# Kernel optimization log

Measured on AMD Instinct MI355X. Metric: run time of the kernel, lower is better.

## Reference

```python
import jax, jax.numpy as jnp
import numpy as np

HID = 2048      # hidden_size
NH = 32         # num_heads
G = 8           # num_kv_groups
R = NH // G     # repeat factor (heads per kv group)
HD = HID // NH  # head_dim = 64
SCALE = HD ** 0.5


def setup_inputs() -> dict:
    key = jax.random.key(0)
    ks = jax.random.split(key, 10)
    B, S = 2, 1024
    x = jax.random.normal(ks[0], (B, S, HID), dtype=jnp.float32)
    attention_mask = jnp.ones((B, S, S), dtype=jnp.float32)
    # Linear params stored as [in, out] (y = x @ W + b), same math as torch Linear.
    Wq = jax.random.normal(ks[1], (HID, HID), dtype=jnp.float32) * 0.02
    bq = jnp.zeros((HID,), dtype=jnp.float32)
    Wk = jax.random.normal(ks[2], (HID, G * HD), dtype=jnp.float32) * 0.02
    bk = jnp.zeros((G * HD,), dtype=jnp.float32)
    Wv = jax.random.normal(ks[3], (HID, G * HD), dtype=jnp.float32) * 0.02
    bv = jnp.zeros((G * HD,), dtype=jnp.float32)
    Wo = jax.random.normal(ks[4], (HID, HID), dtype=jnp.float32) * 0.02
    bo = jnp.zeros((HID,), dtype=jnp.float32)
    return {"x": x, "attention_mask": attention_mask,
            "Wq": Wq, "bq": bq, "Wk": Wk, "bk": bk,
            "Wv": Wv, "bv": bv, "Wo": Wo, "bo": bo}


def reference(x, attention_mask, Wq, bq, Wk, bk, Wv, bv, Wo, bo):
    B, S, _ = x.shape
    # Projections. Group heads as (G, R) instead of repeat_interleave:
    # repeat_interleave(key, R, dim=2) duplicates each kv group R times, which is
    # exactly sharing key[:, :, g] across the R heads of group g.
    q = (x @ Wq + bq).reshape(B, S, G, R, HD)   # [B,S,G,R,HD] (heads = G*R in order)
    k = (x @ Wk + bk).reshape(B, S, G, HD)      # [B,S,G,HD]
    v = (x @ Wv + bv).reshape(B, S, G, HD)
    # scores [B,G,R,Sq,Sk] == torch's [B, NH, Sq, Sk] with NH = G*R
    scores = jnp.einsum('bqgrd,bkgd->bgrqk', q, k) / SCALE
    scores = scores * attention_mask[:, None, None]  # multiplicative mask per head
    w = jax.nn.softmax(scores, axis=-1)
    out = jnp.einsum('bgrqk,bkgd->bqgrd', w, v).reshape(B, S, HID)
    return out @ Wo + bo + x
```

## Files before the change

### kernel.cpp

```cpp
#include <hip/hip_runtime.h>

typedef unsigned short u16;
typedef unsigned int u32;
typedef __attribute__((ext_vector_type(8))) short bf16x8;
typedef __attribute__((ext_vector_type(4))) float f32x4;

#define HID 2048
#define S_LEN 1024
#define BATCH 2
#define G_KV 8
#define R_REP 4
#define HD 64
#define NQKV 3072

__device__ __forceinline__ u16 f2bf(float f) {
    union { u32 u; float ff; } x; x.ff = f;
    u32 u = x.u;
    u += 0x7FFFu + ((u >> 16) & 1u);
    return (u16)(u >> 16);
}
__device__ __forceinline__ float bf2f(u16 v) {
    union { u32 u; float f; } x; x.u = ((u32)v) << 16; return x.f;
}

__device__ __forceinline__ void gload_lds16(const void* g, void* l) {
    __builtin_amdgcn_global_load_lds((const __attribute__((address_space(1))) void*)g,
                                     (__attribute__((address_space(3))) void*)l,
                                     16, 0, 0);
}

__global__ __launch_bounds__(256) void cvt_x(const float* __restrict__ in,
                                             u16* __restrict__ out) {
    int i = (blockIdx.x * 256 + threadIdx.x) * 8;
    float4 a = *(const float4*)(in + i);
    float4 b = *(const float4*)(in + i + 4);
    u16 t[8] = {f2bf(a.x), f2bf(a.y), f2bf(a.z), f2bf(a.w),
                f2bf(b.x), f2bf(b.y), f2bf(b.z), f2bf(b.w)};
    *(uint4*)(out + i) = *(const uint4*)t;
}

__global__ __launch_bounds__(256) void mask_perm(const float* __restrict__ mask,
                                                 u16* __restrict__ out) {
    __shared__ float tile[64 * 68];
    int bid = blockIdx.x;
    int kt = bid & 15, qblk = (bid >> 4) & 15, b = bid >> 8;
    int t = threadIdx.x;
    int row = t >> 2, c0 = (t & 3) * 16;
    const float* src = mask + ((size_t)b * S_LEN + qblk * 64 + row) * S_LEN + kt * 64 + c0;
#pragma unroll
    for (int i = 0; i < 4; ++i)
        *(float4*)&tile[row * 68 + c0 + i * 4] = *(const float4*)(src + i * 4);
    __syncthreads();
    int w = t >> 6, quad = (t >> 4) & 3, l16 = t & 15;
    int prow = w * 16 + quad * 4;
    u16 v[16];
#pragma unroll
    for (int nt = 0; nt < 4; ++nt)
#pragma unroll
        for (int reg = 0; reg < 4; ++reg)
            v[nt * 4 + reg] = f2bf(tile[(prow + reg) * 68 + nt * 16 + l16]);
    u16* dst = out + ((size_t)bid) * 4096 + t * 16;
    *(uint4*)dst = ((uint4*)v)[0];
    *(uint4*)(dst + 8) = ((uint4*)v)[1];
}

__global__ __launch_bounds__(256) void transpose_qkv(const float* __restrict__ Wq,
                                                     const float* __restrict__ Wk,
                                                     const float* __restrict__ Wv,
                                                     u16* __restrict__ out) {
    __shared__ float tile[32][33];
    int n0 = blockIdx.x * 32, k0 = blockIdx.y * 32;
    const float* in; int N, nc0;
    if (n0 < 2048)      { in = Wq; N = 2048; nc0 = n0; }
    else if (n0 < 2560) { in = Wk; N = 512;  nc0 = n0 - 2048; }
    else                { in = Wv; N = 512;  nc0 = n0 - 2560; }
    int tx = threadIdx.x, ty = threadIdx.y;
#pragma unroll
    for (int j = 0; j < 4; ++j)
        tile[ty + j * 8][tx] = in[(size_t)(k0 + ty + j * 8) * N + nc0 + tx];
    __syncthreads();
#pragma unroll
    for (int j = 0; j < 4; ++j)
        out[(size_t)(n0 + ty + j * 8) * 2048 + k0 + tx] = f2bf(tile[tx][ty + j * 8]);
}

__global__ __launch_bounds__(256) void transpose_cvt(const float* __restrict__ in,
                                                     u16* __restrict__ out,
                                                     int K, int N) {
    __shared__ float tile[32][33];
    int n0 = blockIdx.x * 32, k0 = blockIdx.y * 32;
    int tx = threadIdx.x, ty = threadIdx.y;
#pragma unroll
    for (int j = 0; j < 4; ++j)
        tile[ty + j * 8][tx] = in[(size_t)(k0 + ty + j * 8) * N + n0 + tx];
    __syncthreads();
#pragma unroll
    for (int j = 0; j < 4; ++j)
        out[(size_t)(n0 + ty + j * 8) * K + k0 + tx] = f2bf(tile[tx][ty + j * 8]);
}

__global__ __launch_bounds__(256) void gemm_qkv(const u16* __restrict__ Xb,
                                                const u16* __restrict__ WT,
                                                const float* __restrict__ bq,
                                                const float* __restrict__ bk,
                                                const float* __restrict__ bv,
                                                u16* __restrict__ qb,
                                                u16* __restrict__ kb,
                                                u16* __restrict__ vb) {
    __shared__ __align__(16) u16 As[64 * 32];
    __shared__ __align__(16) u16 Bs[128 * 32];
    int tid = threadIdx.x;
    int w = tid >> 6, lane = tid & 63, quad = lane >> 4, l16 = lane & 15;
    int m0 = blockIdx.y * 64, n0 = blockIdx.x * 128;
    int wr = (w >> 1) * 32, wc = (w & 1) * 64;
    int srow = lane >> 2, scol = (lane & 3) * 8;

    f32x4 acc[2][4];
#pragma unroll
    for (int i = 0; i < 2; ++i)
#pragma unroll
        for (int j = 0; j < 4; ++j) acc[i][j] = (f32x4){0.f, 0.f, 0.f, 0.f};

    for (int k0 = 0; k0 < 2048; k0 += 32) {
        gload_lds16(&Xb[(size_t)(m0 + w * 16 + srow) * 2048 + k0 + scol], &As[(w * 16) * 32]);
#pragma unroll
        for (int c = 0; c < 2; ++c) {
            int row = w * 32 + c * 16;
            gload_lds16(&WT[(size_t)(n0 + row + srow) * 2048 + k0 + scol], &Bs[row * 32]);
        }
        __syncthreads();
        bf16x8 af[2], bfr[4];
#pragma unroll
        for (int mt = 0; mt < 2; ++mt)
            af[mt] = *(const bf16x8*)&As[(wr + mt * 16 + l16) * 32 + quad * 8];
#pragma unroll
        for (int nt = 0; nt < 4; ++nt)
            bfr[nt] = *(const bf16x8*)&Bs[(wc + nt * 16 + l16) * 32 + quad * 8];
#pragma unroll
        for (int mt = 0; mt < 2; ++mt)
#pragma unroll
            for (int nt = 0; nt < 4; ++nt)
                acc[mt][nt] = __builtin_amdgcn_mfma_f32_16x16x32_bf16(af[mt], bfr[nt], acc[mt][nt], 0, 0, 0);
        __syncthreads();
    }

#pragma unroll
    for (int nt = 0; nt < 4; ++nt) {
        int n = n0 + wc + nt * 16 + l16;
        float bias;
        if (n < 2048) bias = bq[n];
        else if (n < 2560) bias = bk[n - 2048];
        else bias = bv[n - 2560];
#pragma unroll
        for (int mt = 0; mt < 2; ++mt) {
#pragma unroll
            for (int reg = 0; reg < 4; ++reg) {
                int m = m0 + wr + mt * 16 + quad * 4 + reg;
                float val = acc[mt][nt][reg] + bias;
                int b = m >> 10, s = m & 1023;
                if (n < 2048) {
                    int g = n >> 8, r = (n >> 6) & 3, d = n & 63;
                    qb[((((size_t)(b * G_KV + g) * R_REP + r) * S_LEN) + s) * HD + d] = f2bf(val * 0.125f);
                } else if (n < 2560) {
                    int n2 = n - 2048, g = n2 >> 6, d = n2 & 63;
                    kb[(((size_t)(b * G_KV + g) * S_LEN) + s) * HD + d] = f2bf(val);
                } else {
                    int n2 = n - 2560, g = n2 >> 6, d = n2 & 63;
                    vb[(((size_t)(b * G_KV + g) * HD + d) * S_LEN) + s] = f2bf(val);
                }
            }
        }
    }
}

__global__ __launch_bounds__(256) void attn_mfma(const u16* __restrict__ qbuf,
                                                 const u16* __restrict__ kbuf,
                                                 const u16* __restrict__ vtbuf,
                                                 const u16* __restrict__ mask_pm,
                                                 u16* __restrict__ aout) {
    __shared__ __align__(16) u16 Ks[64 * 72];
    __shared__ __align__(16) u16 Vs[64 * 72];
    __shared__ __align__(16) u16 Ps[64 * 72];

    int d = blockIdx.x;
    int xcd = d & 7, j = d >> 3;
    int pr = xcd * 2 + (j >> 6);
    int r = (j >> 4) & 3, qblk = j & 15;
    int b = pr >> 3, g = pr & 7;

    int tid = threadIdx.x;
    int w = tid >> 6, lane = tid & 63, quad = lane >> 4, l16 = lane & 15;
    int s0 = qblk * 64;

    const u16* qrow = qbuf +
        ((((size_t)(b * G_KV + g) * R_REP + r) * S_LEN) + s0 + w * 16 + l16) * HD;
    bf16x8 qf0 = *(const bf16x8*)(qrow + quad * 8);
    bf16x8 qf1 = *(const bf16x8*)(qrow + 32 + quad * 8);

    f32x4 o_acc[4];
#pragma unroll
    for (int i = 0; i < 4; ++i) o_acc[i] = (f32x4){0.f, 0.f, 0.f, 0.f};
    float l_tot[4] = {0.f, 0.f, 0.f, 0.f};

    const u16* kbase  = kbuf  + (size_t)(b * G_KV + g) * S_LEN * HD;
    const u16* vtbase = vtbuf + (size_t)(b * G_KV + g) * HD * S_LEN;
    const u16* mbase  = mask_pm + ((size_t)(b * 16 + qblk) * 16) * 4096 + tid * 16;

    int srow = tid >> 2, sc = (tid & 3) * 16;
    int prow = w * 16 + quad * 4;

    uint4 kp0, kp1, vp0, vp1, mp0, mp1;
    {
        const u16* kr = kbase + (size_t)srow * HD + sc;
        kp0 = *(const uint4*)kr; kp1 = *(const uint4*)(kr + 8);
        const u16* vr = vtbase + (size_t)srow * S_LEN + sc;
        vp0 = *(const uint4*)vr; vp1 = *(const uint4*)(vr + 8);
        mp0 = *(const uint4*)mbase; mp1 = *(const uint4*)(mbase + 8);
    }

    for (int kt = 0; kt < 16; ++kt) {
        __syncthreads();
        *(uint4*)&Ks[srow * 72 + sc]     = kp0;
        *(uint4*)&Ks[srow * 72 + sc + 8] = kp1;
        *(uint4*)&Vs[srow * 72 + sc]     = vp0;
        *(uint4*)&Vs[srow * 72 + sc + 8] = vp1;
        uint4 m0c = mp0, m1c = mp1;
        __syncthreads();

        if (kt < 15) {
            int nk = (kt + 1) * 64;
            const u16* kr = kbase + (size_t)(nk + srow) * HD + sc;
            kp0 = *(const uint4*)kr; kp1 = *(const uint4*)(kr + 8);
            const u16* vr = vtbase + (size_t)srow * S_LEN + nk + sc;
            vp0 = *(const uint4*)vr; vp1 = *(const uint4*)(vr + 8);
            const u16* mr = mbase + (size_t)(kt + 1) * 4096;
            mp0 = *(const uint4*)mr; mp1 = *(const uint4*)(mr + 8);
        }

        f32x4 p[4];
#pragma unroll
        for (int nt = 0; nt < 4; ++nt) {
            bf16x8 kf0 = *(const bf16x8*)&Ks[(nt * 16 + l16) * 72 + quad * 8];
            bf16x8 kf1 = *(const bf16x8*)&Ks[(nt * 16 + l16) * 72 + 32 + quad * 8];
            f32x4 z = (f32x4){0.f, 0.f, 0.f, 0.f};
            z = __builtin_amdgcn_mfma_f32_16x16x32_bf16(qf0, kf0, z, 0, 0, 0);
            p[nt] = __builtin_amdgcn_mfma_f32_16x16x32_bf16(qf1, kf1, z, 0, 0, 0);
        }

        const u16* mv0 = (const u16*)&m0c;
        const u16* mv1 = (const u16*)&m1c;
        float part[4] = {0.f, 0.f, 0.f, 0.f};
#pragma unroll
        for (int nt = 0; nt < 4; ++nt) {
#pragma unroll
            for (int reg = 0; reg < 4; ++reg) {
                int idx = nt * 4 + reg;
                float m = bf2f(idx < 8 ? mv0[idx] : mv1[idx - 8]);
                float e = __expf(p[nt][reg] * m);
                part[reg] += e;
                Ps[(prow + reg) * 72 + nt * 16 + l16] = f2bf(e);
            }
        }
        __syncthreads();

#pragma unroll
        for (int reg = 0; reg < 4; ++reg) {
            float v = part[reg];
            v += __shfl_xor(v, 1);
            v += __shfl_xor(v, 2);
            v += __shfl_xor(v, 4);
            v += __shfl_xor(v, 8);
            l_tot[reg] += v;
        }

        bf16x8 pf0 = *(const bf16x8*)&Ps[(w * 16 + l16) * 72 + quad * 8];
        bf16x8 pf1 = *(const bf16x8*)&Ps[(w * 16 + l16) * 72 + 32 + quad * 8];
#pragma unroll
        for (int nt = 0; nt < 4; ++nt) {
            bf16x8 vf0 = *(const bf16x8*)&Vs[(nt * 16 + l16) * 72 + quad * 8];
            bf16x8 vf1 = *(const bf16x8*)&Vs[(nt * 16 + l16) * 72 + 32 + quad * 8];
            o_acc[nt] = __builtin_amdgcn_mfma_f32_16x16x32_bf16(pf0, vf0, o_acc[nt], 0, 0, 0);
            o_acc[nt] = __builtin_amdgcn_mfma_f32_16x16x32_bf16(pf1, vf1, o_acc[nt], 0, 0, 0);
        }
    }

#pragma unroll
    for (int reg = 0; reg < 4; ++reg) {
        int row = prow + reg;
        float inv = 1.0f / l_tot[reg];
        int sidx = s0 + row;
        u16* dst = aout + ((size_t)(b * S_LEN + sidx)) * HID + (g * R_REP + r) * HD;
#pragma unroll
        for (int nt = 0; nt < 4; ++nt)
            dst[nt * 16 + l16] = f2bf(o_acc[nt][reg] * inv);
    }
}

__global__ __launch_bounds__(256) void gemm_o(const u16* __restrict__ A,
                                              const u16* __restrict__ WT,
                                              const float* __restrict__ bo,
                                              const float* __restrict__ Xres,
                                              float* __restrict__ out) {
    __shared__ __align__(16) u16 As[64 * 32];
    __shared__ __align__(16) u16 Bs[128 * 32];
    int tid = threadIdx.x;
    int w = tid >> 6, lane = tid & 63, quad = lane >> 4, l16 = lane & 15;
    int m0 = blockIdx.y * 64, n0 = blockIdx.x * 128;
    int wr = (w >> 1) * 32, wc = (w & 1) * 64;
    int srow = lane >> 2, scol = (lane & 3) * 8;

    f32x4 acc[2][4];
#pragma unroll
    for (int i = 0; i < 2; ++i)
#pragma unroll
        for (int j = 0; j < 4; ++j) acc[i][j] = (f32x4){0.f, 0.f, 0.f, 0.f};

    for (int k0 = 0; k0 < 2048; k0 += 32) {
        gload_lds16(&A[(size_t)(m0 + w * 16 + srow) * 2048 + k0 + scol], &As[(w * 16) * 32]);
#pragma unroll
        for (int c = 0; c < 2; ++c) {
            int row = w * 32 + c * 16;
            gload_lds16(&WT[(size_t)(n0 + row + srow) * 2048 + k0 + scol], &Bs[row * 32]);
        }
        __syncthreads();
        bf16x8 af[2], bfr[4];
#pragma unroll
        for (int mt = 0; mt < 2; ++mt)
            af[mt] = *(const bf16x8*)&As[(wr + mt * 16 + l16) * 32 + quad * 8];
#pragma unroll
        for (int nt = 0; nt < 4; ++nt)
            bfr[nt] = *(const bf16x8*)&Bs[(wc + nt * 16 + l16) * 32 + quad * 8];
#pragma unroll
        for (int mt = 0; mt < 2; ++mt)
#pragma unroll
            for (int nt = 0; nt < 4; ++nt)
                acc[mt][nt] = __builtin_amdgcn_mfma_f32_16x16x32_bf16(af[mt], bfr[nt], acc[mt][nt], 0, 0, 0);
        __syncthreads();
    }

#pragma unroll
    for (int nt = 0; nt < 4; ++nt) {
        int n = n0 + wc + nt * 16 + l16;
        float bias = bo[n];
#pragma unroll
        for (int mt = 0; mt < 2; ++mt) {
#pragma unroll
            for (int reg = 0; reg < 4; ++reg) {
                int m = m0 + wr + mt * 16 + quad * 4 + reg;
                out[(size_t)m * 2048 + n] = acc[mt][nt][reg] + bias + Xres[(size_t)m * 2048 + n];
            }
        }
    }
}

extern "C" void kernel_launch(void* const* d_in, const int* in_sizes, int n_in,
                              void* d_out, int out_size, void* d_ws, size_t ws_size,
                              hipStream_t stream) {
    const float* x    = (const float*)d_in[0];
    const float* mask = (const float*)d_in[1];
    const float* Wq   = (const float*)d_in[2];
    const float* bq   = (const float*)d_in[3];
    const float* Wk   = (const float*)d_in[4];
    const float* bk   = (const float*)d_in[5];
    const float* Wv   = (const float*)d_in[6];
    const float* bv   = (const float*)d_in[7];
    const float* Wo   = (const float*)d_in[8];
    const float* bo   = (const float*)d_in[9];
    float* out = (float*)d_out;

    u16* ws = (u16*)d_ws;
    size_t off = 0;
    u16* WqkvT = ws + off; off += (size_t)NQKV * 2048;
    u16* WoT   = ws + off; off += (size_t)2048 * 2048;
    u16* q_buf = ws + off; off += (size_t)BATCH * G_KV * R_REP * S_LEN * HD;
    u16* k_buf = ws + off; off += (size_t)BATCH * G_KV * S_LEN * HD;
    u16* v_buf = ws + off; off += (size_t)BATCH * G_KV * S_LEN * HD;
    u16* a_out = ws + off; off += (size_t)2048 * 2048;
    u16* Xb      = a_out;
    u16* mask_pm = WqkvT;

    cvt_x<<<dim3(2048 * 2048 / (256 * 8)), 256, 0, stream>>>(x, Xb);

    dim3 tb(32, 8);
    transpose_qkv<<<dim3(96, 64), tb, 0, stream>>>(Wq, Wk, Wv, WqkvT);
    transpose_cvt<<<dim3(64, 64), tb, 0, stream>>>(Wo, WoT, 2048, 2048);

    gemm_qkv<<<dim3(NQKV / 128, 2048 / 64), 256, 0, stream>>>(Xb, WqkvT, bq, bk, bv,
                                                              q_buf, k_buf, v_buf);

    mask_perm<<<dim3(BATCH * 16 * 16), 256, 0, stream>>>(mask, mask_pm);

    attn_mfma<<<dim3(BATCH * G_KV * R_REP * (S_LEN / 64)), 256, 0, stream>>>(
        q_buf, k_buf, v_buf, mask_pm, a_out);

    gemm_o<<<dim3(2048 / 128, 2048 / 64), 256, 0, stream>>>(a_out, WoT, bo, x, out);
}
```

Measured before the change: 249.4 us.

## Compute transposed S tile so P is written packed without intra-block barrier

The QK^T MFMA now swaps operands so each lane holds scores for one query row across four consecutive keys. This lets the exp results be rounded and packed into bf16 pairs and written to LDS with one 8-byte store per tile instead of scalar stores. The per-iteration row-sum shuffles go away: each lane accumulates a private partial, which is reduced once at the end through shuffles and a small LDS array, and the __syncthreads before reading P is dropped because each wave only reads its own rows. The mask is kept as fp32 in the new permuted layout, which doubles mask traffic and register use. The end-of-kernel LDS read of row sums has no barrier, which is safe only if each wave reads only the rows it wrote.

```diff
diff --git a/kernel.cpp b/kernel.cpp
--- a/kernel.cpp
+++ b/kernel.cpp
@@ -18,9 +18,6 @@
     u32 u = x.u;
     u += 0x7FFFu + ((u >> 16) & 1u);
     return (u16)(u >> 16);
-}
-__device__ __forceinline__ float bf2f(u16 v) {
-    union { u32 u; float f; } x; x.u = ((u32)v) << 16; return x.f;
 }
 
 __device__ __forceinline__ void gload_lds16(const void* g, void* l) {
@@ -40,7 +37,7 @@
 }
 
 __global__ __launch_bounds__(256) void mask_perm(const float* __restrict__ mask,
-                                                 u16* __restrict__ out) {
+                                                 float* __restrict__ out) {
     __shared__ float tile[64 * 68];
     int bid = blockIdx.x;
     int kt = bid & 15, qblk = (bid >> 4) & 15, b = bid >> 8;
@@ -52,16 +49,13 @@
         *(float4*)&tile[row * 68 + c0 + i * 4] = *(const float4*)(src + i * 4);
     __syncthreads();
     int w = t >> 6, quad = (t >> 4) & 3, l16 = t & 15;
-    int prow = w * 16 + quad * 4;
-    u16 v[16];
-#pragma unroll
-    for (int nt = 0; nt < 4; ++nt)
-#pragma unroll
-        for (int reg = 0; reg < 4; ++reg)
-            v[nt * 4 + reg] = f2bf(tile[(prow + reg) * 68 + nt * 16 + l16]);
-    u16* dst = out + ((size_t)bid) * 4096 + t * 16;
-    *(uint4*)dst = ((uint4*)v)[0];
-    *(uint4*)(dst + 8) = ((uint4*)v)[1];
+    int q = w * 16 + l16;
+    float* dst = out + (size_t)bid * 4096 + t * 16;
+#pragma unroll
+    for (int mt = 0; mt < 4; ++mt) {
+        float4 v = *(const float4*)&tile[q * 68 + mt * 16 + quad * 4];
+        *(float4*)(dst + mt * 4) = v;
+    }
 }
 
 __global__ __launch_bounds__(256) void transpose_qkv(const float* __restrict__ Wq,
@@ -176,11 +170,12 @@
 __global__ __launch_bounds__(256) void attn_mfma(const u16* __restrict__ qbuf,
                                                  const u16* __restrict__ kbuf,
                                                  const u16* __restrict__ vtbuf,
-                                                 const u16* __restrict__ mask_pm,
+                                                 const float* __restrict__ mask_pm,
                                                  u16* __restrict__ aout) {
     __shared__ __align__(16) u16 Ks[64 * 72];
     __shared__ __align__(16) u16 Vs[64 * 72];
     __shared__ __align__(16) u16 Ps[64 * 72];
+    __shared__ float l_lds[64];
 
     int d = blockIdx.x;
     int xcd = d & 7, j = d >> 3;
@@ -191,31 +186,33 @@
     int tid = threadIdx.x;
     int w = tid >> 6, lane = tid & 63, quad = lane >> 4, l16 = lane & 15;
     int s0 = qblk * 64;
+    int q = w * 16 + l16;
 
     const u16* qrow = qbuf +
-        ((((size_t)(b * G_KV + g) * R_REP + r) * S_LEN) + s0 + w * 16 + l16) * HD;
+        ((((size_t)(b * G_KV + g) * R_REP + r) * S_LEN) + s0 + q) * HD;
     bf16x8 qf0 = *(const bf16x8*)(qrow + quad * 8);
     bf16x8 qf1 = *(const bf16x8*)(qrow + 32 + quad * 8);
 
     f32x4 o_acc[4];
 #pragma unroll
     for (int i = 0; i < 4; ++i) o_acc[i] = (f32x4){0.f, 0.f, 0.f, 0.f};
-    float l_tot[4] = {0.f, 0.f, 0.f, 0.f};
+    float l_part = 0.f;
 
     const u16* kbase  = kbuf  + (size_t)(b * G_KV + g) * S_LEN * HD;
     const u16* vtbase = vtbuf + (size_t)(b * G_KV + g) * HD * S_LEN;
-    const u16* mbase  = mask_pm + ((size_t)(b * 16 + qblk) * 16) * 4096 + tid * 16;
+    const float* mbase = mask_pm + ((size_t)(b * 16 + qblk) * 16) * 4096 + tid * 16;
 
     int srow = tid >> 2, sc = (tid & 3) * 16;
-    int prow = w * 16 + quad * 4;
-
-    uint4 kp0, kp1, vp0, vp1, mp0, mp1;
+
+    uint4 kp0, kp1, vp0, vp1;
+    f32x4 mc[4], mn[4];
     {
         const u16* kr = kbase + (size_t)srow * HD + sc;
         kp0 = *(const uint4*)kr; kp1 = *(const uint4*)(kr + 8);
         const u16* vr = vtbase + (size_t)srow * S_LEN + sc;
         vp0 = *(const uint4*)vr; vp1 = *(const uint4*)(vr + 8);
-        mp0 = *(const uint4*)mbase; mp1 = *(const uint4*)(mbase + 8);
+#pragma unroll
+        for (int i = 0; i < 4; ++i) mc[i] = *(const f32x4*)(mbase + i * 4);
     }
 
     for (int kt = 0; kt < 16; ++kt) {
@@ -224,7 +221,6 @@
         *(uint4*)&Ks[srow * 72 + sc + 8] = kp1;
         *(uint4*)&Vs[srow * 72 + sc]     = vp0;
         *(uint4*)&Vs[srow * 72 + sc + 8] = vp1;
-        uint4 m0c = mp0, m1c = mp1;
         __syncthreads();
 
         if (kt < 15) {
@@ -233,48 +229,35 @@
             kp0 = *(const uint4*)kr; kp1 = *(const uint4*)(kr + 8);
             const u16* vr = vtbase + (size_t)srow * S_LEN + nk + sc;
             vp0 = *(const uint4*)vr; vp1 = *(const uint4*)(vr + 8);
-            const u16* mr = mbase + (size_t)(kt + 1) * 4096;
-            mp0 = *(const uint4*)mr; mp1 = *(const uint4*)(mr + 8);
-        }
-
-        f32x4 p[4];
-#pragma unroll
-        for (int nt = 0; nt < 4; ++nt) {
-            bf16x8 kf0 = *(const bf16x8*)&Ks[(nt * 16 + l16) * 72 + quad * 8];
-            bf16x8 kf1 = *(const bf16x8*)&Ks[(nt * 16 + l16) * 72 + 32 + quad * 8];
+            const float* mr = mbase + (size_t)(kt + 1) * 4096;
+#pragma unroll
+            for (int i = 0; i < 4; ++i) mn[i] = *(const f32x4*)(mr + i * 4);
+        }
+
+#pragma unroll
+        for (int mt = 0; mt < 4; ++mt) {
+            bf16x8 af0 = *(const bf16x8*)&Ks[(mt * 16 + l16) * 72 + quad * 8];
+            bf16x8 af1 = *(const bf16x8*)&Ks[(mt * 16 + l16) * 72 + 32 + quad * 8];
             f32x4 z = (f32x4){0.f, 0.f, 0.f, 0.f};
-            z = __builtin_amdgcn_mfma_f32_16x16x32_bf16(qf0, kf0, z, 0, 0, 0);
-            p[nt] = __builtin_amdgcn_mfma_f32_16x16x32_bf16(qf1, kf1, z, 0, 0, 0);
-        }
-
-        const u16* mv0 = (const u16*)&m0c;
-        const u16* mv1 = (const u16*)&m1c;
-        float part[4] = {0.f, 0.f, 0.f, 0.f};
-#pragma unroll
-        for (int nt = 0; nt < 4; ++nt) {
-#pragma unroll
-            for (int reg = 0; reg < 4; ++reg) {
-                int idx = nt * 4 + reg;
-                float m = bf2f(idx < 8 ? mv0[idx] : mv1[idx - 8]);
-                float e = __expf(p[nt][reg] * m);
-                part[reg] += e;
-                Ps[(prow + reg) * 72 + nt * 16 + l16] = f2bf(e);
+            z = __builtin_amdgcn_mfma_f32_16x16x32_bf16(af0, qf0, z, 0, 0, 0);
+            f32x4 s = __builtin_amdgcn_mfma_f32_16x16x32_bf16(af1, qf1, s = z, 0, 0, 0);
+
+            u32 er[4];
+#pragma unroll
+            for (int rg = 0; rg < 4; ++rg) {
+                float e = __expf(s[rg] * mc[mt][rg]);
+                u32 u = __float_as_uint(e) + 0x8000u;
+                er[rg] = u;
+                l_part += __uint_as_float(u & 0xFFFF0000u);
             }
-        }
-        __syncthreads();
-
-#pragma unroll
-        for (int reg = 0; reg < 4; ++reg) {
-            float v = part[reg];
-            v += __shfl_xor(v, 1);
-            v += __shfl_xor(v, 2);
-            v += __shfl_xor(v, 4);
-            v += __shfl_xor(v, 8);
-            l_tot[reg] += v;
-        }
-
-        bf16x8 pf0 = *(const bf16x8*)&Ps[(w * 16 + l16) * 72 + quad * 8];
-        bf16x8 pf1 = *(const bf16x8*)&Ps[(w * 16 + l16) * 72 + 32 + quad * 8];
+            uint2 pk;
+            pk.x = __builtin_amdgcn_perm(er[1], er[0], 0x07060302u);
+            pk.y = __builtin_amdgcn_perm(er[3], er[2], 0x07060302u);
+            *(uint2*)&Ps[q * 72 + mt * 16 + quad * 4] = pk;
+        }
+
+        bf16x8 pf0 = *(const bf16x8*)&Ps[q * 72 + quad * 8];
+        bf16x8 pf1 = *(const bf16x8*)&Ps[q * 72 + 32 + quad * 8];
 #pragma unroll
         for (int nt = 0; nt < 4; ++nt) {
             bf16x8 vf0 = *(const bf16x8*)&Vs[(nt * 16 + l16) * 72 + quad * 8];
@@ -282,12 +265,18 @@
             o_acc[nt] = __builtin_amdgcn_mfma_f32_16x16x32_bf16(pf0, vf0, o_acc[nt], 0, 0, 0);
             o_acc[nt] = __builtin_amdgcn_mfma_f32_16x16x32_bf16(pf1, vf1, o_acc[nt], 0, 0, 0);
         }
-    }
+#pragma unroll
+        for (int i = 0; i < 4; ++i) mc[i] = mn[i];
+    }
+
+    l_part += __shfl_xor(l_part, 16);
+    l_part += __shfl_xor(l_part, 32);
+    l_lds[w * 16 + l16] = l_part;
 
 #pragma unroll
     for (int reg = 0; reg < 4; ++reg) {
-        int row = prow + reg;
-        float inv = 1.0f / l_tot[reg];
+        int row = w * 16 + quad * 4 + reg;
+        float inv = 1.0f / l_lds[row];
         int sidx = s0 + row;
         u16* dst = aout + ((size_t)(b * S_LEN + sidx)) * HID + (g * R_REP + r) * HD;
 #pragma unroll
@@ -376,8 +365,8 @@
     u16* k_buf = ws + off; off += (size_t)BATCH * G_KV * S_LEN * HD;
     u16* v_buf = ws + off; off += (size_t)BATCH * G_KV * S_LEN * HD;
     u16* a_out = ws + off; off += (size_t)2048 * 2048;
-    u16* Xb      = a_out;
-    u16* mask_pm = WqkvT;
+    u16* Xb       = a_out;
+    float* mask_pm = (float*)WqkvT;
 
     cvt_x<<<dim3(2048 * 2048 / (256 * 8)), 256, 0, stream>>>(x, Xb);
 
```

New measurement: 242.2 us. 2.9% less time.
